# Kernel optimization log

Hardware: AMD Instinct MI355X
Metric: run time of the kernel (lower is better)

Reference implementation:

```python
import jax, jax.numpy as jnp
import numpy as np

# R2D2-style NghSampler2 config
NGH, SUBQ, SUBD, POS_D, NEG_D, BORDER, SUBD_NEG = 7, 8, 1, 3, 5, 16, 8

def _make_offsets():
    rad = (NGH // SUBD) * NGH
    pos, neg = [], []
    for j in range(-rad, rad + 1, SUBD):
        for i in range(-rad, rad + 1, SUBD):
            d2 = i * i + j * j
            if d2 <= POS_D ** 2:
                pos.append((i, j))
            elif NEG_D ** 2 <= d2 <= NGH ** 2:
                neg.append((i, j))
    # rows: [x(i), y(j)], matching torch .view(-1,2).t()
    return np.array(pos, np.int32).T, np.array(neg, np.int32).T

POS_OFF, NEG_OFF = _make_offsets()  # [2,29], [2,80]

def _grid(B, H, W, step):
    xs = np.arange(BORDER, W - BORDER, step)
    ys = np.arange(BORDER, H - BORDER, step)
    H1, W1 = len(ys), len(xs)
    b1 = np.repeat(np.arange(B), H1 * W1)
    y1 = np.tile(np.repeat(ys, W1), B)
    x1 = np.tile(np.tile(xs, H1), B)
    return b1, y1, x1, (B, H1, W1)

def setup_inputs() -> dict:
    key = jax.random.key(0)
    k1, k2, k3, k4, k5 = jax.random.split(key, 5)
    B, C, H, W = 4, 128, 256, 256
    feat1 = jax.random.normal(k1, (B, C, H, W), jnp.float32)
    feat2 = jax.random.normal(k2, (B, C, H, W), jnp.float32)
    conf1 = jax.random.uniform(k3, (B, 1, H, W), jnp.float32)
    conf2 = jax.random.uniform(k4, (B, 1, H, W), jnp.float32)
    aflow = jax.random.uniform(k5, (B, 2, H, W), jnp.float32) * (W - 1)
    return {"feat1": feat1, "feat2": feat2, "conf1": conf1, "conf2": conf2, "aflow": aflow}

def reference(feat1, feat2, conf1, conf2, aflow):
    B, C, H, W = feat1.shape
    b1n, y1n, x1n, shape = _grid(B, H, W, SUBQ)
    b1, y1, x1 = jnp.asarray(b1n), jnp.asarray(y1n), jnp.asarray(x1n)
    pos_off, neg_off = jnp.asarray(POS_OFF), jnp.asarray(NEG_OFF)

    f1 = feat1[b1, :, y1, x1]                      # [Q,C] query descriptors
    qconf = conf1[b1, 0, y1, x1].reshape(shape)    # [B,H1,W1]
    xy2 = (aflow[b1, :, y1, x1] + 0.5).astype(jnp.int32).T  # [2,Q] (x,y)
    mask = ((xy2[0] >= 0) & (xy2[1] >= 0) & (xy2[0] < W) & (xy2[1] < H)).reshape(shape)

    def clamp(xy):
        return jnp.stack([jnp.clip(xy[0], 0, W - 1), jnp.clip(xy[1], 0, H - 1)])

    # positives: gather feat2 at GT-correspondence + pos offsets, dot with f1
    xy2p = clamp(xy2[:, None, :] + pos_off[:, :, None])      # [2,P,Q]
    f2p = feat2[b1, :, xy2p[1], xy2p[0]]                     # [P,Q,C]
    ps_all = jnp.einsum('qc,pqc->qp', f1, f2p)               # [Q,P]
    pscores = ps_all.max(axis=1, keepdims=True)              # [Q,1]
    pos = jnp.argmax(ps_all, axis=1)                         # [Q]
    sel = clamp(xy2 + pos_off[:, pos])                       # [2,Q]
    qconf = (qconf + conf2[b1, 0, sel[1], sel[0]].reshape(shape)) / 2

    # negatives: ring of offsets around GT correspondence
    xy2n = clamp(xy2[:, None, :] + neg_off[:, :, None])      # [2,N,Q]
    f2n = feat2[b1, :, xy2n[1], xy2n[0]]                     # [N,Q,C]
    nscores = jnp.einsum('qc,nqc->qn', f1, f2n)              # [Q,N]

    # distractors on a regular grid in image 2
    b3n, y3n, x3n, _ = _grid(B, H, W, SUBD_NEG)
    b3, y3, x3 = jnp.asarray(b3n), jnp.asarray(y3n), jnp.asarray(x3n)
    distractors = feat2[b3, :, y3, x3]                       # [Q2,C]
    dscores = f1 @ distractors.T                             # [Q,Q2]
    dis2 = (x3[None, :] - xy2[0][:, None]) ** 2 \
         + (y3[None, :] - xy2[1][:, None]) ** 2 \
         + (b3[None, :] != b1[:, None]).astype(jnp.int32) * NEG_D ** 2
    dscores = jnp.where(dis2 < NEG_D ** 2, 0.0, dscores)

    scores = jnp.concatenate([pscores, nscores, dscores], axis=1)
    npos = pscores.shape[1]
    gt = jnp.concatenate([
        jnp.ones((scores.shape[0], npos), jnp.uint8),
        jnp.zeros((scores.shape[0], scores.shape[1] - npos), jnp.uint8)], axis=1)
    return scores, gt, mask, qconf
```

## Files before the change

kernel.cpp:

```cpp
#include <hip/hip_runtime.h>

#define CCH   128
#define HH    256
#define WW    256
#define BB    4
#define H1    28
#define W1    28
#define QTOT  3136
#define NPOS  29
#define NNEG  80
#define NDIS  3136
#define SCOLS 3217

typedef short s8v __attribute__((ext_vector_type(8)));
typedef float f4v __attribute__((ext_vector_type(4)));

__device__ __forceinline__ unsigned short f2bf(float f) {
  unsigned int u = __float_as_uint(f);
  u += 0x7fffu + ((u >> 16) & 1u);
  return (unsigned short)(u >> 16);
}
__device__ __forceinline__ float bf2f(unsigned short h) {
  return __uint_as_float(((unsigned int)h) << 16);
}

__constant__ int POS_I[NPOS] = {
  0, -2,-1,0,1,2, -2,-1,0,1,2, -3,-2,-1,0,1,2,3, -2,-1,0,1,2, -2,-1,0,1,2, 0};
__constant__ int POS_J[NPOS] = {
  -3, -2,-2,-2,-2,-2, -1,-1,-1,-1,-1, 0,0,0,0,0,0,0, 1,1,1,1,1, 2,2,2,2,2, 3};
__constant__ int NEG_I[NNEG] = {
  0, -3,-2,-1,0,1,2,3, -4,-3,-2,-1,0,1,2,3,4, -5,-4,-3,3,4,5, -6,-5,-4,4,5,6,
  -6,-5,5,6, -6,-5,5,6, -7,-6,-5,5,6,7, -6,-5,5,6, -6,-5,5,6, -6,-5,-4,4,5,6,
  -5,-4,-3,3,4,5, -4,-3,-2,-1,0,1,2,3,4, -3,-2,-1,0,1,2,3, 0};
__constant__ int NEG_J[NNEG] = {
  -7, -6,-6,-6,-6,-6,-6,-6, -5,-5,-5,-5,-5,-5,-5,-5,-5, -4,-4,-4,-4,-4,-4,
  -3,-3,-3,-3,-3,-3, -2,-2,-2,-2, -1,-1,-1,-1, 0,0,0,0,0,0, 1,1,1,1, 2,2,2,2,
  3,3,3,3,3,3, 4,4,4,4,4,4, 5,5,5,5,5,5,5,5,5, 6,6,6,6,6,6,6, 7};

__global__ void zerogt_kernel(float4* __restrict__ gt4, int n4) {
  int i = blockIdx.x * blockDim.x + threadIdx.x;
  if (i < n4) gt4[i] = make_float4(0.f, 0.f, 0.f, 0.f);
}

__global__ void transpose_kernel(const float* __restrict__ feat2,
                                 unsigned short* __restrict__ feat2T) {
  __shared__ unsigned short tile[CCH][33];
  int x0 = blockIdx.x * 32;
  int y  = blockIdx.y;
  int b  = blockIdx.z;
  int tid = threadIdx.x;
  const float* src = feat2 + ((size_t)b * CCH * HH + y) * WW;
  #pragma unroll
  for (int it = 0; it < 16; ++it) {
    int idx = it * 256 + tid;
    int c = idx >> 5, xi = idx & 31;
    tile[c][xi] = f2bf(src[(size_t)c * HH * WW + x0 + xi]);
  }
  __syncthreads();
  int xi = tid >> 3, cg = (tid & 7) * 16;
  __align__(16) unsigned short tmp[16];
  #pragma unroll
  for (int k = 0; k < 16; ++k) tmp[k] = tile[cg + k][xi];
  unsigned short* dst = feat2T + ((size_t)((b * HH + y) * WW) + x0 + xi) * CCH + cg;
  *(uint4*)dst       = *(const uint4*)tmp;
  *(uint4*)(dst + 8) = *(const uint4*)(tmp + 8);
}

__global__ void gather_kernel(const float* __restrict__ feat1,
                              const unsigned short* __restrict__ feat2T,
                              const float* __restrict__ aflow,
                              unsigned short* __restrict__ F1bf,
                              unsigned short* __restrict__ F2bf,
                              int* __restrict__ X2, int* __restrict__ Y2,
                              float* __restrict__ mask_out) {
  int q = blockIdx.x, c = threadIdx.x;
  int b = q / (H1 * W1), r = q % (H1 * W1);
  int y = 16 + 8 * (r / W1);
  int x = 16 + 8 * (r % W1);
  F1bf[(size_t)q * CCH + c] = f2bf(feat1[((size_t)(b * CCH + c) * HH + y) * WW + x]);
  F2bf[(size_t)q * CCH + c] = feat2T[((size_t)((b * HH + y) * WW) + x) * CCH + c];
  if (c == 0) {
    float ax = aflow[((size_t)(b * 2 + 0) * HH + y) * WW + x];
    float ay = aflow[((size_t)(b * 2 + 1) * HH + y) * WW + x];
    int x2 = (int)(ax + 0.5f);
    int y2 = (int)(ay + 0.5f);
    X2[q] = x2; Y2[q] = y2;
    mask_out[q] = (x2 >= 0 && y2 >= 0 && x2 < WW && y2 < HH) ? 1.0f : 0.0f;
  }
}

__global__ void posneg_kernel(const unsigned short* __restrict__ feat2T,
                              const float* __restrict__ conf1,
                              const float* __restrict__ conf2,
                              const unsigned short* __restrict__ F1bf,
                              const int* __restrict__ X2, const int* __restrict__ Y2,
                              float* __restrict__ scores, float* __restrict__ gt,
                              float* __restrict__ qconf_out) {
  __shared__ float posv[NPOS];
  __shared__ float negv[NNEG];
  __shared__ float bestv;
  int q = blockIdx.x;
  int t = threadIdx.x;
  int w = t >> 6, lane = t & 63;
  int b = q / (H1 * W1), r = q % (H1 * W1);
  int y = 16 + 8 * (r / W1);
  int x = 16 + 8 * (r % W1);

  unsigned int f1p = ((const unsigned int*)(F1bf + (size_t)q * CCH))[lane];
  float f1a = __uint_as_float(f1p << 16);
  float f1b = __uint_as_float(f1p & 0xffff0000u);
  int x2 = X2[q], y2 = Y2[q];

  for (int off = w; off < NPOS + NNEG; off += 4) {
    int di = (off < NPOS) ? POS_I[off] : NEG_I[off - NPOS];
    int dj = (off < NPOS) ? POS_J[off] : NEG_J[off - NPOS];
    int xk = min(max(x2 + di, 0), WW - 1);
    int yk = min(max(y2 + dj, 0), HH - 1);
    unsigned int v = ((const unsigned int*)(feat2T +
        ((size_t)((b * HH + yk) * WW) + xk) * CCH))[lane];
    float s = f1a * __uint_as_float(v << 16)
            + f1b * __uint_as_float(v & 0xffff0000u);
    #pragma unroll
    for (int o = 32; o > 0; o >>= 1) s += __shfl_xor(s, o);
    if (lane == 0) {
      if (off < NPOS) posv[off] = s;
      else            negv[off - NPOS] = s;
    }
  }
  __syncthreads();

  if (t == 0) {
    float best = posv[0]; int bi = 0;
    for (int k = 1; k < NPOS; ++k)
      if (posv[k] > best) { best = posv[k]; bi = k; }
    bestv = best;
    int sx = min(max(x2 + POS_I[bi], 0), WW - 1);
    int sy = min(max(y2 + POS_J[bi], 0), HH - 1);
    float c1 = conf1[((size_t)b * HH + y) * WW + x];
    float c2 = conf2[((size_t)b * HH + sy) * WW + sx];
    qconf_out[q] = 0.5f * (c1 + c2);
    gt[(size_t)q * SCOLS] = 1.0f;
  }
  __syncthreads();

  if (t < 1 + NNEG)
    scores[(size_t)q * SCOLS + t] = (t == 0) ? bestv : negv[t - 1];
}

__global__ void dscore_kernel(const unsigned short* __restrict__ F1bf,
                              const unsigned short* __restrict__ F2bf,
                              const int* __restrict__ X2, const int* __restrict__ Y2,
                              float* __restrict__ scores) {
  __shared__ float tile[64][66];
  int w = threadIdx.x >> 6, lane = threadIdx.x & 63;
  int qb = blockIdx.y * 64;
  int db = blockIdx.x * 64;
  int m  = lane & 15;
  int ko = (lane >> 4) * 8;

  f4v acc[4];
  #pragma unroll
  for (int dt = 0; dt < 4; ++dt) acc[dt] = (f4v){0.f, 0.f, 0.f, 0.f};

  #pragma unroll
  for (int kk = 0; kk < 4; ++kk) {
    s8v a = *(const s8v*)(F1bf + (size_t)(qb + w * 16 + m) * CCH + kk * 32 + ko);
    #pragma unroll
    for (int dt = 0; dt < 4; ++dt) {
      s8v bfr = *(const s8v*)(F2bf + (size_t)(db + dt * 16 + m) * CCH + kk * 32 + ko);
      acc[dt] = __builtin_amdgcn_mfma_f32_16x16x32_bf16(a, bfr, acc[dt], 0, 0, 0);
    }
  }

  int rbase = (lane >> 4) * 4, col = lane & 15;
  #pragma unroll
  for (int dt = 0; dt < 4; ++dt)
    #pragma unroll
    for (int r = 0; r < 4; ++r)
      tile[w * 16 + rbase + r][dt * 16 + col] = acc[dt][r];
  __syncthreads();

  int d = db + lane;
  int dbat = d / (H1 * W1), dr = d % (H1 * W1);
  int dy = 16 + 8 * (dr / W1), dx = 16 + 8 * (dr % W1);

  #pragma unroll
  for (int i = 0; i < 16; ++i) {
    int row = w * 16 + i;
    int q = qb + row;
    int x2 = X2[q], y2 = Y2[q];
    int qbat = q / (H1 * W1);
    int ddx = dx - x2, ddy = dy - y2;
    int dis2 = ddx * ddx + ddy * ddy + (dbat != qbat ? 25 : 0);
    float v = tile[row][lane];
    if (dis2 < 25) v = 0.f;
    scores[(size_t)q * SCOLS + 1 + NNEG + d] = v;
  }
}

extern "C" void kernel_launch(void* const* d_in, const int* in_sizes, int n_in,
                              void* d_out, int out_size, void* d_ws, size_t ws_size,
                              hipStream_t stream) {
  const float* feat1 = (const float*)d_in[0];
  const float* feat2 = (const float*)d_in[1];
  const float* conf1 = (const float*)d_in[2];
  const float* conf2 = (const float*)d_in[3];
  const float* aflow = (const float*)d_in[4];

  float* out       = (float*)d_out;
  float* scores    = out;
  float* gt        = out + (size_t)QTOT * SCOLS;
  float* mask_out  = out + 2 * (size_t)QTOT * SCOLS;
  float* qconf_out = mask_out + QTOT;

  unsigned short* feat2T = (unsigned short*)d_ws;
  unsigned short* F1bf   = feat2T + (size_t)BB * HH * WW * CCH;
  unsigned short* F2bf   = F1bf + (size_t)QTOT * CCH;
  int* X2 = (int*)(F2bf + (size_t)QTOT * CCH);
  int* Y2 = X2 + QTOT;

  int n4 = (QTOT * SCOLS) / 4;
  zerogt_kernel<<<(n4 + 255) / 256, 256, 0, stream>>>((float4*)gt, n4);
  dim3 gT(WW / 32, HH, BB);
  transpose_kernel<<<gT, 256, 0, stream>>>(feat2, feat2T);
  gather_kernel<<<QTOT, CCH, 0, stream>>>(feat1, feat2T, aflow, F1bf, F2bf, X2, Y2, mask_out);
  posneg_kernel<<<QTOT, 256, 0, stream>>>(feat2T, conf1, conf2, F1bf, X2, Y2, scores, gt, qconf_out);
  dim3 gD(NDIS / 64, QTOT / 64);
  dscore_kernel<<<gD, 256, 0, stream>>>(F1bf, F2bf, X2, Y2, scores);
}
```

Before: 375.3 us.

## Fuse gt zeroing and gathers into producer kernels, drop separate launches

Removes the standalone gt-zeroing kernel by having posneg write the first 81 gt columns and dscore write zeros alongside scores. The F2 distractor gather moves into the transpose kernel and the F1/flow gather into posneg, eliminating a launch and a pass over memory. Posneg is restructured so each thread pair computes one offset's dot product with 128-bit loads against fp32 f1 held in shared memory, instead of a wavefront-wide shuffle reduction. Keeping f1 in fp32 for pos/neg scores changes rounding slightly, and the dscore epilogue now issues twice the stores.

Measured after the change: 339.7 us. 9.5% less time.

```diff
diff --git a/kernel.cpp b/kernel.cpp
--- a/kernel.cpp
+++ b/kernel.cpp
@@ -20,9 +20,8 @@
   u += 0x7fffu + ((u >> 16) & 1u);
   return (unsigned short)(u >> 16);
 }
-__device__ __forceinline__ float bf2f(unsigned short h) {
-  return __uint_as_float(((unsigned int)h) << 16);
-}
+__device__ __forceinline__ float bflo(unsigned int v) { return __uint_as_float(v << 16); }
+__device__ __forceinline__ float bfhi(unsigned int v) { return __uint_as_float(v & 0xffff0000u); }
 
 __constant__ int POS_I[NPOS] = {
   0, -2,-1,0,1,2, -2,-1,0,1,2, -3,-2,-1,0,1,2,3, -2,-1,0,1,2, -2,-1,0,1,2, 0};
@@ -37,13 +36,9 @@
   -3,-3,-3,-3,-3,-3, -2,-2,-2,-2, -1,-1,-1,-1, 0,0,0,0,0,0, 1,1,1,1, 2,2,2,2,
   3,3,3,3,3,3, 4,4,4,4,4,4, 5,5,5,5,5,5,5,5,5, 6,6,6,6,6,6,6, 7};
 
-__global__ void zerogt_kernel(float4* __restrict__ gt4, int n4) {
-  int i = blockIdx.x * blockDim.x + threadIdx.x;
-  if (i < n4) gt4[i] = make_float4(0.f, 0.f, 0.f, 0.f);
-}
-
 __global__ void transpose_kernel(const float* __restrict__ feat2,
-                                 unsigned short* __restrict__ feat2T) {
+                                 unsigned short* __restrict__ feat2T,
+                                 unsigned short* __restrict__ F2bf) {
   __shared__ unsigned short tile[CCH][33];
   int x0 = blockIdx.x * 32;
   int y  = blockIdx.y;
@@ -64,69 +59,82 @@
   unsigned short* dst = feat2T + ((size_t)((b * HH + y) * WW) + x0 + xi) * CCH + cg;
   *(uint4*)dst       = *(const uint4*)tmp;
   *(uint4*)(dst + 8) = *(const uint4*)(tmp + 8);
-}
-
-__global__ void gather_kernel(const float* __restrict__ feat1,
+
+  if ((y & 7) == 0 && y >= 16 && y <= 232) {
+    int xs = x0 + (tid >> 6) * 8;
+    if (xs >= 16 && xs <= 232) {
+      int cp = tid & 63;
+      int xi2 = xs - x0;
+      unsigned int lo = tile[2 * cp][xi2], hi = tile[2 * cp + 1][xi2];
+      int q = b * H1 * W1 + ((y - 16) >> 3) * W1 + ((xs - 16) >> 3);
+      ((unsigned int*)(F2bf + (size_t)q * CCH))[cp] = lo | (hi << 16);
+    }
+  }
+}
+
+__global__ void posneg_kernel(const float* __restrict__ feat1,
                               const unsigned short* __restrict__ feat2T,
+                              const float* __restrict__ conf1,
+                              const float* __restrict__ conf2,
                               const float* __restrict__ aflow,
                               unsigned short* __restrict__ F1bf,
-                              unsigned short* __restrict__ F2bf,
                               int* __restrict__ X2, int* __restrict__ Y2,
-                              float* __restrict__ mask_out) {
-  int q = blockIdx.x, c = threadIdx.x;
+                              float* __restrict__ mask_out,
+                              float* __restrict__ scores, float* __restrict__ gt,
+                              float* __restrict__ qconf_out) {
+  __shared__ float f1s[CCH];
+  __shared__ float posv[NPOS];
+  __shared__ float negv[NNEG];
+  __shared__ float bestv;
+  __shared__ int sxy[2];
+  int q = blockIdx.x, t = threadIdx.x;
   int b = q / (H1 * W1), r = q % (H1 * W1);
   int y = 16 + 8 * (r / W1);
   int x = 16 + 8 * (r % W1);
-  F1bf[(size_t)q * CCH + c] = f2bf(feat1[((size_t)(b * CCH + c) * HH + y) * WW + x]);
-  F2bf[(size_t)q * CCH + c] = feat2T[((size_t)((b * HH + y) * WW) + x) * CCH + c];
-  if (c == 0) {
+
+  if (t < CCH) {
+    float v = feat1[((size_t)(b * CCH + t) * HH + y) * WW + x];
+    f1s[t] = v;
+    F1bf[(size_t)q * CCH + t] = f2bf(v);
+  }
+  if (t == 128) {
     float ax = aflow[((size_t)(b * 2 + 0) * HH + y) * WW + x];
     float ay = aflow[((size_t)(b * 2 + 1) * HH + y) * WW + x];
     int x2 = (int)(ax + 0.5f);
     int y2 = (int)(ay + 0.5f);
-    X2[q] = x2; Y2[q] = y2;
+    X2[q] = x2; Y2[q] = y2; sxy[0] = x2; sxy[1] = y2;
     mask_out[q] = (x2 >= 0 && y2 >= 0 && x2 < WW && y2 < HH) ? 1.0f : 0.0f;
   }
-}
-
-__global__ void posneg_kernel(const unsigned short* __restrict__ feat2T,
-                              const float* __restrict__ conf1,
-                              const float* __restrict__ conf2,
-                              const unsigned short* __restrict__ F1bf,
-                              const int* __restrict__ X2, const int* __restrict__ Y2,
-                              float* __restrict__ scores, float* __restrict__ gt,
-                              float* __restrict__ qconf_out) {
-  __shared__ float posv[NPOS];
-  __shared__ float negv[NNEG];
-  __shared__ float bestv;
-  int q = blockIdx.x;
-  int t = threadIdx.x;
-  int w = t >> 6, lane = t & 63;
-  int b = q / (H1 * W1), r = q % (H1 * W1);
-  int y = 16 + 8 * (r / W1);
-  int x = 16 + 8 * (r % W1);
-
-  unsigned int f1p = ((const unsigned int*)(F1bf + (size_t)q * CCH))[lane];
-  float f1a = __uint_as_float(f1p << 16);
-  float f1b = __uint_as_float(f1p & 0xffff0000u);
-  int x2 = X2[q], y2 = Y2[q];
-
-  for (int off = w; off < NPOS + NNEG; off += 4) {
+  __syncthreads();
+  int x2 = sxy[0], y2 = sxy[1];
+
+  if (t < 2 * (NPOS + NNEG)) {
+    int off = t >> 1, half = t & 1;
     int di = (off < NPOS) ? POS_I[off] : NEG_I[off - NPOS];
     int dj = (off < NPOS) ? POS_J[off] : NEG_J[off - NPOS];
     int xk = min(max(x2 + di, 0), WW - 1);
     int yk = min(max(y2 + dj, 0), HH - 1);
-    unsigned int v = ((const unsigned int*)(feat2T +
-        ((size_t)((b * HH + yk) * WW) + xk) * CCH))[lane];
-    float s = f1a * __uint_as_float(v << 16)
-            + f1b * __uint_as_float(v & 0xffff0000u);
+    const uint4* p4 = (const uint4*)(feat2T +
+        ((size_t)((b * HH + yk) * WW) + xk) * CCH + half * 64);
+    float acc = 0.f;
     #pragma unroll
-    for (int o = 32; o > 0; o >>= 1) s += __shfl_xor(s, o);
-    if (lane == 0) {
-      if (off < NPOS) posv[off] = s;
-      else            negv[off - NPOS] = s;
-    }
-  }
+    for (int i = 0; i < 8; ++i) {
+      uint4 v = p4[i];
+      float4 fa = *(const float4*)&f1s[half * 64 + i * 8];
+      float4 fb = *(const float4*)&f1s[half * 64 + i * 8 + 4];
+      acc += fa.x * bflo(v.x) + fa.y * bfhi(v.x)
+           + fa.z * bflo(v.y) + fa.w * bfhi(v.y)
+           + fb.x * bflo(v.z) + fb.y * bfhi(v.z)
+           + fb.z * bflo(v.w) + fb.w * bfhi(v.w);
+    }
+    acc += __shfl_xor(acc, 1);
+    if (half == 0) {
+      if (off < NPOS) posv[off] = acc;
+      else            negv[off - NPOS] = acc;
+    }
+  }
+  if (t < 1 + NNEG)
+    gt[(size_t)q * SCOLS + t] = (t == 0) ? 1.0f : 0.0f;
   __syncthreads();
 
   if (t == 0) {
@@ -139,7 +147,6 @@
     float c1 = conf1[((size_t)b * HH + y) * WW + x];
     float c2 = conf2[((size_t)b * HH + sy) * WW + sx];
     qconf_out[q] = 0.5f * (c1 + c2);
-    gt[(size_t)q * SCOLS] = 1.0f;
   }
   __syncthreads();
 
@@ -150,13 +157,19 @@
 __global__ void dscore_kernel(const unsigned short* __restrict__ F1bf,
                               const unsigned short* __restrict__ F2bf,
                               const int* __restrict__ X2, const int* __restrict__ Y2,
-                              float* __restrict__ scores) {
+                              float* __restrict__ scores, float* __restrict__ gt) {
   __shared__ float tile[64][66];
+  __shared__ int sx2[64], sy2[64];
   int w = threadIdx.x >> 6, lane = threadIdx.x & 63;
   int qb = blockIdx.y * 64;
   int db = blockIdx.x * 64;
   int m  = lane & 15;
   int ko = (lane >> 4) * 8;
+
+  if (threadIdx.x < 64) {
+    sx2[threadIdx.x] = X2[qb + threadIdx.x];
+    sy2[threadIdx.x] = Y2[qb + threadIdx.x];
+  }
 
   f4v acc[4];
   #pragma unroll
@@ -188,13 +201,14 @@
   for (int i = 0; i < 16; ++i) {
     int row = w * 16 + i;
     int q = qb + row;
-    int x2 = X2[q], y2 = Y2[q];
     int qbat = q / (H1 * W1);
-    int ddx = dx - x2, ddy = dy - y2;
+    int ddx = dx - sx2[row], ddy = dy - sy2[row];
     int dis2 = ddx * ddx + ddy * ddy + (dbat != qbat ? 25 : 0);
     float v = tile[row][lane];
     if (dis2 < 25) v = 0.f;
-    scores[(size_t)q * SCOLS + 1 + NNEG + d] = v;
+    size_t o = (size_t)q * SCOLS + 1 + NNEG + d;
+    scores[o] = v;
+    gt[o] = 0.f;
   }
 }
 
@@ -219,12 +233,10 @@
   int* X2 = (int*)(F2bf + (size_t)QTOT * CCH);
   int* Y2 = X2 + QTOT;
 
-  int n4 = (QTOT * SCOLS) / 4;
-  zerogt_kernel<<<(n4 + 255) / 256, 256, 0, stream>>>((float4*)gt, n4);
   dim3 gT(WW / 32, HH, BB);
-  transpose_kernel<<<gT, 256, 0, stream>>>(feat2, feat2T);
-  gather_kernel<<<QTOT, CCH, 0, stream>>>(feat1, feat2T, aflow, F1bf, F2bf, X2, Y2, mask_out);
-  posneg_kernel<<<QTOT, 256, 0, stream>>>(feat2T, conf1, conf2, F1bf, X2, Y2, scores, gt, qconf_out);
+  transpose_kernel<<<gT, 256, 0, stream>>>(feat2, feat2T, F2bf);
+  posneg_kernel<<<QTOT, 256, 0, stream>>>(feat1, feat2T, conf1, conf2, aflow,
+                                          F1bf, X2, Y2, mask_out, scores, gt, qconf_out);
   dim3 gD(NDIS / 64, QTOT / 64);
-  dscore_kernel<<<gD, 256, 0, stream>>>(F1bf, F2bf, X2, Y2, scores);
-}
+  dscore_kernel<<<gD, 256, 0, stream>>>(F1bf, F2bf, X2, Y2, scores, gt);
+}
```
